# Kernel tuning notes

Measured on AMD Instinct MI355X. Metric: run time of the kernel, lower is better.

The kernel has to match this reference:

```python
import jax, jax.numpy as jnp
import numpy as np

B, N, DEG = 128, 2048, 16
E = N * DEG
EMB, D, H, L = 16, 4, 4, 4
DH = D // H  # per-head dim
OBS_DIM = 6154
HID1, HID2, OUT = 45, 45, 15


def setup_inputs() -> dict:
    key = jax.random.key(0)
    ks = iter(jax.random.split(key, 40))
    nrm = lambda shape, s=0.2: jax.random.normal(next(ks), shape, jnp.float32) * s
    inp = {
        "x": nrm((B, N, EMB), 1.0),
        "obs": nrm((B, OBS_DIM), 1.0),
        "src": jax.random.randint(next(ks), (E,), 0, N, jnp.int32),
        "dst": jnp.repeat(jnp.arange(N, dtype=jnp.int32), DEG),  # each node has DEG in-edges
        "agent_nodes": jax.random.randint(next(ks), (B,), 0, N, jnp.int32),
        "We": nrm((EMB, D)), "be": jnp.zeros((D,), jnp.float32),
        "Wq": nrm((L, D, D)), "bq": jnp.zeros((L, D), jnp.float32),
        "Wk": nrm((L, D, D)), "bk": jnp.zeros((L, D), jnp.float32),
        "Wv": nrm((L, D, D)), "bv": jnp.zeros((L, D), jnp.float32),
        "Wo": nrm((L, D, D)), "bo": jnp.zeros((L, D), jnp.float32),
        "ln1_g": jnp.ones((L, D), jnp.float32), "ln1_b": jnp.zeros((L, D), jnp.float32),
        "W1": nrm((L, D, 2 * D)), "b1": jnp.zeros((L, 2 * D), jnp.float32),
        "W2": nrm((L, 2 * D, D)), "b2": jnp.zeros((L, D), jnp.float32),
        "ln2_g": jnp.ones((L, D), jnp.float32), "ln2_b": jnp.zeros((L, D), jnp.float32),
        "oW1": nrm((D + OBS_DIM, HID1), 0.05), "ob1": jnp.zeros((HID1,), jnp.float32),
        "oW2": nrm((HID1, HID2)), "ob2": jnp.zeros((HID2,), jnp.float32),
        "oW3": nrm((HID2, OUT)), "ob3": jnp.zeros((OUT,), jnp.float32),
    }
    return inp


def _ln(x, g, b):
    m = x.mean(-1, keepdims=True)
    v = ((x - m) ** 2).mean(-1, keepdims=True)
    return g * (x - m) * jax.lax.rsqrt(v + 1e-5) + b


def reference(x, obs, src, dst, agent_nodes, We, be, Wq, bq, Wk, bk, Wv, bv, Wo, bo,
              ln1_g, ln1_b, W1, b1, W2, b2, ln2_g, ln2_b, oW1, ob1, oW2, ob2, oW3, ob3):
    inv_sqrt_dh = 1.0 / np.sqrt(DH)

    def per_graph(xg, node):  # xg: [N, EMB], node: scalar agent location
        h = xg @ We + be  # [N, D] node embedding
        for l in range(L):
            q = (h @ Wq[l] + bq[l]).reshape(N, H, DH)
            k = (h @ Wk[l] + bk[l]).reshape(N, H, DH)
            v = (h @ Wv[l] + bv[l]).reshape(N, H, DH)
            # edge-wise attention scores: gather at dst (query) and src (key)
            s = (q[dst] * k[src]).sum(-1) * inv_sqrt_dh  # [E, H]
            m = jax.ops.segment_max(s, dst, num_segments=N)  # [N, H]
            e = jnp.exp(s - m[dst])
            z = jax.ops.segment_sum(e, dst, num_segments=N)
            a = e / (z[dst] + 1e-6)  # softmax over incoming edges
            msg = jax.ops.segment_sum(a[:, :, None] * v[src], dst, num_segments=N)  # [N, H, DH]
            h_attn = msg.reshape(N, D) @ Wo[l] + bo[l]
            h = _ln(h + h_attn, ln1_g[l], ln1_b[l])  # residual + norm
            ffn = jax.nn.relu(h @ W1[l] + b1[l]) @ W2[l] + b2[l]
            h = _ln(h + ffn, ln2_g[l], ln2_b[l])
        return h[node]  # [D] feature at the agent's node

    gat_out = jax.vmap(per_graph)(x, agent_nodes)  # [B, D]
    feat = jnp.concatenate([gat_out, obs], axis=1)  # [B, D + OBS_DIM]
    hmid = jnp.tanh(feat @ oW1 + ob1)
    hmid = jnp.tanh(hmid @ oW2 + ob2)
    logits = hmid @ oW3 + ob3  # [B, OUT]
    return logits
```

## Files before the change

### kernel.cpp

```cpp
#include <hip/hip_runtime.h>
#include <hip/hip_bf16.h>

#define NB 128
#define NN 2048
#define DEG 16
#define EMBD 16
#define NL 4
#define OBSD 6154
#define HID 45
#define NOUT 15
#define KS 16
#define CH 385
#define RPB 4
#define LOG2E 1.44269504f
#define MEGAB NB
#define MLPB ((NB / RPB) * KS)

__device__ __forceinline__ float frcp(float v) { return __builtin_amdgcn_rcpf(v); }

__device__ __forceinline__ uint32_t pk_bf16(float a, float b) {
    uint32_t ua = __float_as_uint(a); ua += 0x7fffu + ((ua >> 16) & 1u);
    uint32_t ub = __float_as_uint(b); ub += 0x7fffu + ((ub >> 16) & 1u);
    return (ua >> 16) | (ub & 0xffff0000u);
}
__device__ __forceinline__ float lo_bf(uint32_t u) { return __uint_as_float(u << 16); }
__device__ __forceinline__ float hi_bf(uint32_t u) { return __uint_as_float(u & 0xffff0000u); }

__device__ __forceinline__ void ln4(const float* p, const float* g, const float* bb, float* o) {
    float m = 0.25f * (p[0] + p[1] + p[2] + p[3]);
    float var = 0.f;
#pragma unroll
    for (int j = 0; j < 4; ++j) { float d = p[j] - m; var += d * d; }
    var *= 0.25f;
    float rs = rsqrtf(var + 1e-5f);
#pragma unroll
    for (int j = 0; j < 4; ++j) o[j] = g[j] * (p[j] - m) * rs + bb[j];
}

__device__ __forceinline__ void node_tail(float* hh, const float* msg,
    const float* wo, const float* bol, const float* g1, const float* be1,
    const float* w1, const float* b1l, const float* w2, const float* b2l,
    const float* g2, const float* be2)
{
    float pre[4];
#pragma unroll
    for (int j = 0; j < 4; ++j) {
        float s = bol[j];
#pragma unroll
        for (int i = 0; i < 4; ++i) s += msg[i] * wo[i * 4 + j];
        pre[j] = hh[j] + s;
    }
    float hn[4];
    ln4(pre, g1, be1, hn);
    float mid[8];
#pragma unroll
    for (int j = 0; j < 8; ++j) {
        float s = b1l[j];
#pragma unroll
        for (int i = 0; i < 4; ++i) s += hn[i] * w1[i * 8 + j];
        mid[j] = fmaxf(s, 0.f);
    }
    float pre2[4];
#pragma unroll
    for (int j = 0; j < 4; ++j) {
        float s = b2l[j];
#pragma unroll
        for (int i = 0; i < 8; ++i) s += mid[i] * w2[i * 4 + j];
        pre2[j] = hn[j] + s;
    }
    ln4(pre2, g2, be2, hh);
}

__device__ __forceinline__ uint4 kv_pack(const float* hh,
    const float* wk, const float* bkl, const float* wv, const float* bvl)
{
    float kk[4], vv[4];
#pragma unroll
    for (int j = 0; j < 4; ++j) {
        float sk = bkl[j], sv = bvl[j];
#pragma unroll
        for (int i = 0; i < 4; ++i) {
            sk += hh[i] * wk[i * 4 + j];
            sv += hh[i] * wv[i * 4 + j];
        }
        kk[j] = sk; vv[j] = sv;
    }
    return make_uint4(pk_bf16(kk[0], kk[1]), pk_bf16(kk[2], kk[3]),
                      pk_bf16(vv[0], vv[1]), pk_bf16(vv[2], vv[3]));
}

__device__ __forceinline__ void gather_tail(const uint4* kv, const int* su,
    const float* q2, float* hh, int l,
    const float* Wo, const float* bo, const float* ln1_g, const float* ln1_b,
    const float* W1, const float* b1, const float* W2, const float* b2,
    const float* ln2_g, const float* ln2_b)
{
    float z[4] = {0.f, 0.f, 0.f, 0.f}, wa[4] = {0.f, 0.f, 0.f, 0.f};
#pragma unroll
    for (int eb = 0; eb < 4; ++eb) {
        uint4 t0 = kv[su[eb * 4 + 0]];
        uint4 t1 = kv[su[eb * 4 + 1]];
        uint4 t2 = kv[su[eb * 4 + 2]];
        uint4 t3 = kv[su[eb * 4 + 3]];
        float p;
        p = __builtin_amdgcn_exp2f(q2[0] * lo_bf(t0.x)); z[0] += p; wa[0] += p * lo_bf(t0.z);
        p = __builtin_amdgcn_exp2f(q2[1] * hi_bf(t0.x)); z[1] += p; wa[1] += p * hi_bf(t0.z);
        p = __builtin_amdgcn_exp2f(q2[2] * lo_bf(t0.y)); z[2] += p; wa[2] += p * lo_bf(t0.w);
        p = __builtin_amdgcn_exp2f(q2[3] * hi_bf(t0.y)); z[3] += p; wa[3] += p * hi_bf(t0.w);
        p = __builtin_amdgcn_exp2f(q2[0] * lo_bf(t1.x)); z[0] += p; wa[0] += p * lo_bf(t1.z);
        p = __builtin_amdgcn_exp2f(q2[1] * hi_bf(t1.x)); z[1] += p; wa[1] += p * hi_bf(t1.z);
        p = __builtin_amdgcn_exp2f(q2[2] * lo_bf(t1.y)); z[2] += p; wa[2] += p * lo_bf(t1.w);
        p = __builtin_amdgcn_exp2f(q2[3] * hi_bf(t1.y)); z[3] += p; wa[3] += p * hi_bf(t1.w);
        p = __builtin_amdgcn_exp2f(q2[0] * lo_bf(t2.x)); z[0] += p; wa[0] += p * lo_bf(t2.z);
        p = __builtin_amdgcn_exp2f(q2[1] * hi_bf(t2.x)); z[1] += p; wa[1] += p * hi_bf(t2.z);
        p = __builtin_amdgcn_exp2f(q2[2] * lo_bf(t2.y)); z[2] += p; wa[2] += p * lo_bf(t2.w);
        p = __builtin_amdgcn_exp2f(q2[3] * hi_bf(t2.y)); z[3] += p; wa[3] += p * hi_bf(t2.w);
        p = __builtin_amdgcn_exp2f(q2[0] * lo_bf(t3.x)); z[0] += p; wa[0] += p * lo_bf(t3.z);
        p = __builtin_amdgcn_exp2f(q2[1] * hi_bf(t3.x)); z[1] += p; wa[1] += p * hi_bf(t3.z);
        p = __builtin_amdgcn_exp2f(q2[2] * lo_bf(t3.y)); z[2] += p; wa[2] += p * lo_bf(t3.w);
        p = __builtin_amdgcn_exp2f(q2[3] * hi_bf(t3.y)); z[3] += p; wa[3] += p * hi_bf(t3.w);
    }
    float msg[4];
#pragma unroll
    for (int j = 0; j < 4; ++j) msg[j] = wa[j] * frcp(z[j] + 1e-6f);
    node_tail(hh, msg, Wo + l * 16, bo + l * 4, ln1_g + l * 4, ln1_b + l * 4,
              W1 + l * 32, b1 + l * 8, W2 + l * 32, b2 + l * 4,
              ln2_g + l * 4, ln2_b + l * 4);
}

__device__ __forceinline__ void mlp1_block(int mb, int tid,
    const float* __restrict__ obs, const float* __restrict__ oW1,
    float* __restrict__ partial, float* red)
{
    const int rg = mb >> 4;
    const int ks = mb & (KS - 1);
    const int w = tid >> 6, lane = tid & 63;
    const int c0 = ks * CH;
    const int c1 = min(c0 + CH, OBSD);
    const int wl = (c1 - c0 + 15) >> 4;
    const int s0 = c0 + w * wl;
    const int s1 = min(s0 + wl, c1);
    const float* ob0 = obs + (size_t)(rg * RPB) * OBSD;

    if (lane < HID) {
        float acc[RPB] = {0.f, 0.f, 0.f, 0.f};
        for (int i = s0; i < s1; ++i) {
            float wv = oW1[(size_t)(i + 4) * HID + lane];
#pragma unroll
            for (int r = 0; r < RPB; ++r)
                acc[r] += ob0[(size_t)r * OBSD + i] * wv;
        }
#pragma unroll
        for (int r = 0; r < RPB; ++r) red[(w * RPB + r) * HID + lane] = acc[r];
    }
    __syncthreads();
    for (int idx = tid; idx < RPB * HID; idx += 1024) {
        const int r = idx / HID, j = idx % HID;
        float s = 0.f;
#pragma unroll
        for (int ww = 0; ww < 16; ++ww) s += red[(ww * RPB + r) * HID + j];
        partial[(size_t)((rg * RPB + r) * KS + ks) * HID + j] = s;
    }
}

__global__ __launch_bounds__(1024) void fused_kernel(
    const float* __restrict__ x, const int* __restrict__ src,
    const int* __restrict__ agent_nodes,
    const float* __restrict__ obs, const float* __restrict__ oW1,
    float* __restrict__ partial, float* __restrict__ gat_out,
    const float* __restrict__ We, const float* __restrict__ be,
    const float* __restrict__ Wq, const float* __restrict__ bq,
    const float* __restrict__ Wk, const float* __restrict__ bk,
    const float* __restrict__ Wv, const float* __restrict__ bv,
    const float* __restrict__ Wo, const float* __restrict__ bo,
    const float* __restrict__ ln1_g, const float* __restrict__ ln1_b,
    const float* __restrict__ W1, const float* __restrict__ b1,
    const float* __restrict__ W2, const float* __restrict__ b2,
    const float* __restrict__ ln2_g, const float* __restrict__ ln2_b)
{
    __shared__ uint4  kvbuf[NN];
    __shared__ float4 h1lds[NN];
    __shared__ int    conen[289];
    __shared__ float  h2c[289][4];
    __shared__ float  h3buf[17][4];
    const int bid = blockIdx.x;
    const int tid = threadIdx.x;

    if (bid >= MEGAB) {
        mlp1_block(bid - MEGAB, tid, obs, oW1, partial,
                   reinterpret_cast<float*>(kvbuf));
        return;
    }

    const int b = bid;
    const int ag = agent_nodes[b];

    if (tid < 17)  conen[tid] = (tid < 16) ? src[ag * DEG + tid] : ag;
    if (tid < 272) {
        const int i = tid >> 4, e = tid & 15;
        const int ti = (i < 16) ? src[ag * DEG + i] : ag;
        conen[17 + tid] = src[ti * DEG + e];
    }

    float he[2][4];
#pragma unroll
    for (int c = 0; c < 2; ++c) {
        const int n = c * 1024 + tid;
        const float4* xr = reinterpret_cast<const float4*>(
            x + ((size_t)b * NN + n) * EMBD);
        float xv[16];
#pragma unroll
        for (int t4 = 0; t4 < 4; ++t4) {
            float4 t = xr[t4];
            xv[t4 * 4 + 0] = t.x; xv[t4 * 4 + 1] = t.y;
            xv[t4 * 4 + 2] = t.z; xv[t4 * 4 + 3] = t.w;
        }
#pragma unroll
        for (int j = 0; j < 4; ++j) {
            float s = be[j];
#pragma unroll
            for (int i = 0; i < 16; ++i) s += xv[i] * We[i * 4 + j];
            he[c][j] = s;
        }
        kvbuf[n] = kv_pack(he[c], Wk, bk, Wv, bv);
    }
    __syncthreads();

    float h1r[2][4];
#pragma unroll
    for (int u = 0; u < 2; ++u) {
        const int n = u * 1024 + tid;
        float q2[4];
#pragma unroll
        for (int j = 0; j < 4; ++j) {
            float sq = bq[j];
#pragma unroll
            for (int i = 0; i < 4; ++i) sq += he[u][i] * Wq[i * 4 + j];
            q2[j] = sq * LOG2E;
        }
        int su[16];
        const int4* sp = reinterpret_cast<const int4*>(src + n * DEG);
#pragma unroll
        for (int t4 = 0; t4 < 4; ++t4) {
            int4 s4 = sp[t4];
            su[t4 * 4 + 0] = s4.x; su[t4 * 4 + 1] = s4.y;
            su[t4 * 4 + 2] = s4.z; su[t4 * 4 + 3] = s4.w;
        }
        float hh[4] = {he[u][0], he[u][1], he[u][2], he[u][3]};
        gather_tail(kvbuf, su, q2, hh, 0, Wo, bo, ln1_g, ln1_b, W1, b1, W2, b2,
                    ln2_g, ln2_b);
#pragma unroll
        for (int j = 0; j < 4; ++j) h1r[u][j] = hh[j];
    }
    __syncthreads();

    {
        const float* wk1 = Wk + 16; const float* bk1 = bk + 4;
        const float* wv1 = Wv + 16; const float* bv1 = bv + 4;
#pragma unroll
        for (int u = 0; u < 2; ++u) {
            const int n = u * 1024 + tid;
            kvbuf[n] = kv_pack(h1r[u], wk1, bk1, wv1, bv1);
            h1lds[n] = make_float4(h1r[u][0], h1r[u][1], h1r[u][2], h1r[u][3]);
        }
    }
    __syncthreads();

    if (tid < 289) {
        const int node = conen[tid];
        float4 hn4 = h1lds[node];
        float hh[4] = {hn4.x, hn4.y, hn4.z, hn4.w};
        float q2[4];
        {
            const float* wq = Wq + 16; const float* bql = bq + 4;
#pragma unroll
            for (int j = 0; j < 4; ++j) {
                float sq = bql[j];
#pragma unroll
                for (int i = 0; i < 4; ++i) sq += hh[i] * wq[i * 4 + j];
                q2[j] = sq * LOG2E;
            }
        }
        int su2[16];
        const int4* sp = reinterpret_cast<const int4*>(src + node * DEG);
#pragma unroll
        for (int t4 = 0; t4 < 4; ++t4) {
            int4 s4 = sp[t4];
            su2[t4 * 4 + 0] = s4.x; su2[t4 * 4 + 1] = s4.y;
            su2[t4 * 4 + 2] = s4.z; su2[t4 * 4 + 3] = s4.w;
        }
        gather_tail(kvbuf, su2, q2, hh, 1, Wo, bo, ln1_g, ln1_b, W1, b1, W2, b2,
                    ln2_g, ln2_b);
#pragma unroll
        for (int j = 0; j < 4; ++j) h2c[tid][j] = hh[j];
    }
    __syncthreads();

    if (tid < 272) {
        const int i = tid >> 4, e = tid & 15;
        const int l2 = 2;
        float q2[4];
        {
            const float* wq = Wq + l2 * 16; const float* bql = bq + l2 * 4;
#pragma unroll
            for (int j = 0; j < 4; ++j) {
                float sq = bql[j];
#pragma unroll
                for (int k = 0; k < 4; ++k) sq += h2c[i][k] * wq[k * 4 + j];
                q2[j] = sq * LOG2E;
            }
        }
        const float* hnb = h2c[17 + tid];
        float z[4], pv[4];
        {
            const float* wk = Wk + l2 * 16; const float* bkl = bk + l2 * 4;
            const float* wv = Wv + l2 * 16; const float* bvl = bv + l2 * 4;
#pragma unroll
            for (int j = 0; j < 4; ++j) {
                float kh = bkl[j], vh = bvl[j];
#pragma unroll
                for (int k = 0; k < 4; ++k) {
                    kh += hnb[k] * wk[k * 4 + j];
                    vh += hnb[k] * wv[k * 4 + j];
                }
                float p = __builtin_amdgcn_exp2f(q2[j] * kh);
                z[j] = p; pv[j] = p * vh;
            }
        }
#pragma unroll
        for (int m = 1; m <= 8; m <<= 1) {
#pragma unroll
            for (int j = 0; j < 4; ++j) {
                z[j]  += __shfl_xor(z[j], m, 64);
                pv[j] += __shfl_xor(pv[j], m, 64);
            }
        }
        if (e == 0) {
            float msg[4];
#pragma unroll
            for (int j = 0; j < 4; ++j) msg[j] = pv[j] * frcp(z[j] + 1e-6f);
            float hh[4] = {h2c[i][0], h2c[i][1], h2c[i][2], h2c[i][3]};
            node_tail(hh, msg, Wo + l2 * 16, bo + l2 * 4, ln1_g + l2 * 4, ln1_b + l2 * 4,
                      W1 + l2 * 32, b1 + l2 * 8, W2 + l2 * 32, b2 + l2 * 4,
                      ln2_g + l2 * 4, ln2_b + l2 * 4);
#pragma unroll
            for (int j = 0; j < 4; ++j) h3buf[i][j] = hh[j];
        }
    }
    __syncthreads();

    if (tid < 64) {
        const int e = tid >> 2, hd = tid & 3;
        const int l3 = 3;
        float ha[4] = {h3buf[16][0], h3buf[16][1], h3buf[16][2], h3buf[16][3]};
        float qh;
        {
            const float* wq = Wq + l3 * 16;
            qh = bq[l3 * 4 + hd];
#pragma unroll
            for (int i = 0; i < 4; ++i) qh += ha[i] * wq[i * 4 + hd];
            qh *= LOG2E;
        }
        float kh, vh;
        {
            const float* wk3 = Wk + l3 * 16; const float* wv3 = Wv + l3 * 16;
            kh = bk[l3 * 4 + hd]; vh = bv[l3 * 4 + hd];
#pragma unroll
            for (int i = 0; i < 4; ++i) {
                kh += h3buf[e][i] * wk3[i * 4 + hd];
                vh += h3buf[e][i] * wv3[i * 4 + hd];
            }
        }
        float p = __builtin_amdgcn_exp2f(qh * kh);
        float z = p, wv_s = p * vh;
#pragma unroll
        for (int m = 4; m <= 32; m <<= 1) {
            z    += __shfl_xor(z, m, 64);
            wv_s += __shfl_xor(wv_s, m, 64);
        }
        float msg_h = wv_s * frcp(z + 1e-6f);
        float msg[4];
#pragma unroll
        for (int j = 0; j < 4; ++j) msg[j] = __shfl(msg_h, (tid & ~3) + j, 64);

        float hh[4] = {ha[0], ha[1], ha[2], ha[3]};
        node_tail(hh, msg, Wo + l3 * 16, bo + l3 * 4, ln1_g + l3 * 4, ln1_b + l3 * 4,
                  W1 + l3 * 32, b1 + l3 * 8, W2 + l3 * 32, b2 + l3 * 4,
                  ln2_g + l3 * 4, ln2_b + l3 * 4);
        if (tid == 0) {
#pragma unroll
            for (int j = 0; j < 4; ++j) gat_out[b * 4 + j] = hh[j];
        }
    }
}

__global__ __launch_bounds__(64) void mlp2_kernel(
    const float* __restrict__ partial, const float* __restrict__ gat,
    const float* __restrict__ oW1, const float* __restrict__ ob1,
    const float* __restrict__ oW2, const float* __restrict__ ob2,
    const float* __restrict__ oW3, const float* __restrict__ ob3,
    float* __restrict__ out)
{
    __shared__ float hm1[HID], hm2[HID];
    const int b = blockIdx.x;
    const int tid = threadIdx.x;
    if (tid < HID) {
        float s = ob1[tid];
        const float* pp = partial + (size_t)b * KS * HID + tid;
#pragma unroll
        for (int ks = 0; ks < KS; ++ks) s += pp[ks * HID];
#pragma unroll
        for (int k = 0; k < 4; ++k) s += gat[b * 4 + k] * oW1[k * HID + tid];
        hm1[tid] = tanhf(s);
    }
    __syncthreads();
    if (tid < HID) {
        float s = ob2[tid];
        for (int k = 0; k < HID; ++k) s += hm1[k] * oW2[k * HID + tid];
        hm2[tid] = tanhf(s);
    }
    __syncthreads();
    if (tid < NOUT) {
        float s = ob3[tid];
        for (int k = 0; k < HID; ++k) s += hm2[k] * oW3[k * NOUT + tid];
        out[(size_t)b * NOUT + tid] = s;
    }
}

__global__ __launch_bounds__(1024) void gat_single_kernel(
    const float* __restrict__ x, const int* __restrict__ src,
    const int* __restrict__ agent_nodes,
    const float* __restrict__ We, const float* __restrict__ be,
    const float* __restrict__ Wq, const float* __restrict__ bq,
    const float* __restrict__ Wk, const float* __restrict__ bk,
    const float* __restrict__ Wv, const float* __restrict__ bv,
    const float* __restrict__ Wo, const float* __restrict__ bo,
    const float* __restrict__ ln1_g, const float* __restrict__ ln1_b,
    const float* __restrict__ W1, const float* __restrict__ b1,
    const float* __restrict__ W2, const float* __restrict__ b2,
    const float* __restrict__ ln2_g, const float* __restrict__ ln2_b,
    float* __restrict__ gat_out)
{
    __shared__ uint4 kv[NN];
    const int b = blockIdx.x;
    const int tid = threadIdx.x;
    float h[2][4];
#pragma unroll
    for (int u = 0; u < 2; ++u) {
        const int n = tid + u * 1024;
        const float4* xr = reinterpret_cast<const float4*>(x + ((size_t)b * NN + n) * EMBD);
        float xv[16];
#pragma unroll
        for (int t4 = 0; t4 < 4; ++t4) {
            float4 t = xr[t4];
            xv[t4 * 4 + 0] = t.x; xv[t4 * 4 + 1] = t.y;
            xv[t4 * 4 + 2] = t.z; xv[t4 * 4 + 3] = t.w;
        }
#pragma unroll
        for (int j = 0; j < 4; ++j) {
            float s = be[j];
#pragma unroll
            for (int i = 0; i < 16; ++i) s += xv[i] * We[i * 4 + j];
            h[u][j] = s;
        }
    }
    for (int l = 0; l < NL; ++l) {
        float q2[2][4];
        const float* wq = Wq + l * 16; const float* bql = bq + l * 4;
        const float* wk = Wk + l * 16; const float* bkl = bk + l * 4;
        const float* wv = Wv + l * 16; const float* bvl = bv + l * 4;
#pragma unroll
        for (int u = 0; u < 2; ++u) {
            const int n = tid + u * 1024;
#pragma unroll
            for (int j = 0; j < 4; ++j) {
                float sq = bql[j];
#pragma unroll
                for (int i = 0; i < 4; ++i) sq += h[u][i] * wq[i * 4 + j];
                q2[u][j] = sq * LOG2E;
            }
            kv[n] = kv_pack(h[u], wk, bkl, wv, bvl);
        }
        __syncthreads();
#pragma unroll
        for (int u = 0; u < 2; ++u) {
            const int n = tid + u * 1024;
            int su[16];
            const int4* sp = reinterpret_cast<const int4*>(src + n * DEG);
#pragma unroll
            for (int t4 = 0; t4 < 4; ++t4) {
                int4 s4 = sp[t4];
                su[t4 * 4 + 0] = s4.x; su[t4 * 4 + 1] = s4.y;
                su[t4 * 4 + 2] = s4.z; su[t4 * 4 + 3] = s4.w;
            }
            gather_tail(kv, su, q2[u], h[u], l, Wo, bo, ln1_g, ln1_b,
                        W1, b1, W2, b2, ln2_g, ln2_b);
        }
        __syncthreads();
    }
    const int agent = agent_nodes[b];
#pragma unroll
    for (int u = 0; u < 2; ++u) {
        if (tid + u * 1024 == agent) {
#pragma unroll
            for (int j = 0; j < 4; ++j) gat_out[b * 4 + j] = h[u][j];
        }
    }
}

__global__ __launch_bounds__(1024) void mlp1_fb_kernel(
    const float* __restrict__ obs, const float* __restrict__ oW1,
    float* __restrict__ partial)
{
    __shared__ float red[16 * RPB * HID];
    mlp1_block(blockIdx.x, threadIdx.x, obs, oW1, partial, red);
}

extern "C" void kernel_launch(void* const* d_in, const int* in_sizes, int n_in,
                              void* d_out, int out_size, void* d_ws, size_t ws_size,
                              hipStream_t stream) {
    const float* x      = (const float*)d_in[0];
    const float* obs    = (const float*)d_in[1];
    const int*   src    = (const int*)d_in[2];
    const int*   agent  = (const int*)d_in[4];
    const float* We     = (const float*)d_in[5];
    const float* be     = (const float*)d_in[6];
    const float* Wq     = (const float*)d_in[7];
    const float* bq     = (const float*)d_in[8];
    const float* Wk     = (const float*)d_in[9];
    const float* bk     = (const float*)d_in[10];
    const float* Wv     = (const float*)d_in[11];
    const float* bv     = (const float*)d_in[12];
    const float* Wo     = (const float*)d_in[13];
    const float* bo     = (const float*)d_in[14];
    const float* ln1_g  = (const float*)d_in[15];
    const float* ln1_b  = (const float*)d_in[16];
    const float* W1     = (const float*)d_in[17];
    const float* b1     = (const float*)d_in[18];
    const float* W2     = (const float*)d_in[19];
    const float* b2     = (const float*)d_in[20];
    const float* ln2_g  = (const float*)d_in[21];
    const float* ln2_b  = (const float*)d_in[22];
    const float* oW1    = (const float*)d_in[23];
    const float* ob1    = (const float*)d_in[24];
    const float* oW2    = (const float*)d_in[25];
    const float* ob2    = (const float*)d_in[26];
    const float* oW3    = (const float*)d_in[27];
    const float* ob3    = (const float*)d_in[28];

    float* out = (float*)d_out;
    char*  ws  = (char*)d_ws;

    float* gat_out = (float*)ws;
    float* partial = (float*)(ws + 2048);
    const size_t need = 2048 + 368640;

    if (ws_size >= need) {
        fused_kernel<<<MEGAB + MLPB, 1024, 0, stream>>>(x, src, agent, obs, oW1,
            partial, gat_out,
            We, be, Wq, bq, Wk, bk, Wv, bv, Wo, bo, ln1_g, ln1_b, W1, b1, W2, b2,
            ln2_g, ln2_b);
        mlp2_kernel<<<NB, 64, 0, stream>>>(partial, gat_out, oW1, ob1, oW2, ob2,
                                           oW3, ob3, out);
    } else {
        gat_single_kernel<<<NB, 1024, 0, stream>>>(x, src, agent, We, be, Wq, bq, Wk, bk,
                                                   Wv, bv, Wo, bo, ln1_g, ln1_b, W1, b1,
                                                   W2, b2, ln2_g, ln2_b, gat_out);
        mlp1_fb_kernel<<<MLPB, 1024, 0, stream>>>(obs, oW1, partial);
        mlp2_kernel<<<NB, 64, 0, stream>>>(partial, gat_out, oW1, ob1, oW2, ob2,
                                           oW3, ob3, out);
    }
}
```

Baseline: 31.46 us.

## Fuse GAT, obs matvec, and output MLP into one single-launch kernel

Merges the GAT graph work, the obs@oW1 matvec and the tanh MLP head into a single 128-block kernel, so the second launch and the workspace round-trip of partial sums are gone. Each graph block now computes its own row's obs dot products across 16 waves, with 4 independent accumulators, while its x loads are in flight. It also hoists the x loads into registers early. The cost is that the separate 512 matvec blocks, which reused oW1 across 4 rows, are dropped, so each block re-reads the full oW1 and has more serial work on only 128 blocks.

```diff
diff --git a/kernel.cpp b/kernel.cpp
--- a/kernel.cpp
+++ b/kernel.cpp
@@ -9,12 +9,9 @@
 #define OBSD 6154
 #define HID 45
 #define NOUT 15
-#define KS 16
-#define CH 385
-#define RPB 4
 #define LOG2E 1.44269504f
-#define MEGAB NB
-#define MLPB ((NB / RPB) * KS)
+#define NW 16
+#define CHW 385
 
 __device__ __forceinline__ float frcp(float v) { return __builtin_amdgcn_rcpf(v); }
 
@@ -128,308 +125,10 @@
               ln2_g + l * 4, ln2_b + l * 4);
 }
 
-__device__ __forceinline__ void mlp1_block(int mb, int tid,
-    const float* __restrict__ obs, const float* __restrict__ oW1,
-    float* __restrict__ partial, float* red)
-{
-    const int rg = mb >> 4;
-    const int ks = mb & (KS - 1);
-    const int w = tid >> 6, lane = tid & 63;
-    const int c0 = ks * CH;
-    const int c1 = min(c0 + CH, OBSD);
-    const int wl = (c1 - c0 + 15) >> 4;
-    const int s0 = c0 + w * wl;
-    const int s1 = min(s0 + wl, c1);
-    const float* ob0 = obs + (size_t)(rg * RPB) * OBSD;
-
-    if (lane < HID) {
-        float acc[RPB] = {0.f, 0.f, 0.f, 0.f};
-        for (int i = s0; i < s1; ++i) {
-            float wv = oW1[(size_t)(i + 4) * HID + lane];
-#pragma unroll
-            for (int r = 0; r < RPB; ++r)
-                acc[r] += ob0[(size_t)r * OBSD + i] * wv;
-        }
-#pragma unroll
-        for (int r = 0; r < RPB; ++r) red[(w * RPB + r) * HID + lane] = acc[r];
-    }
-    __syncthreads();
-    for (int idx = tid; idx < RPB * HID; idx += 1024) {
-        const int r = idx / HID, j = idx % HID;
-        float s = 0.f;
-#pragma unroll
-        for (int ww = 0; ww < 16; ++ww) s += red[(ww * RPB + r) * HID + j];
-        partial[(size_t)((rg * RPB + r) * KS + ks) * HID + j] = s;
-    }
-}
-
-__global__ __launch_bounds__(1024) void fused_kernel(
+__global__ __launch_bounds__(1024) void mega_kernel(
     const float* __restrict__ x, const int* __restrict__ src,
     const int* __restrict__ agent_nodes,
-    const float* __restrict__ obs, const float* __restrict__ oW1,
-    float* __restrict__ partial, float* __restrict__ gat_out,
-    const float* __restrict__ We, const float* __restrict__ be,
-    const float* __restrict__ Wq, const float* __restrict__ bq,
-    const float* __restrict__ Wk, const float* __restrict__ bk,
-    const float* __restrict__ Wv, const float* __restrict__ bv,
-    const float* __restrict__ Wo, const float* __restrict__ bo,
-    const float* __restrict__ ln1_g, const float* __restrict__ ln1_b,
-    const float* __restrict__ W1, const float* __restrict__ b1,
-    const float* __restrict__ W2, const float* __restrict__ b2,
-    const float* __restrict__ ln2_g, const float* __restrict__ ln2_b)
-{
-    __shared__ uint4  kvbuf[NN];
-    __shared__ float4 h1lds[NN];
-    __shared__ int    conen[289];
-    __shared__ float  h2c[289][4];
-    __shared__ float  h3buf[17][4];
-    const int bid = blockIdx.x;
-    const int tid = threadIdx.x;
-
-    if (bid >= MEGAB) {
-        mlp1_block(bid - MEGAB, tid, obs, oW1, partial,
-                   reinterpret_cast<float*>(kvbuf));
-        return;
-    }
-
-    const int b = bid;
-    const int ag = agent_nodes[b];
-
-    if (tid < 17)  conen[tid] = (tid < 16) ? src[ag * DEG + tid] : ag;
-    if (tid < 272) {
-        const int i = tid >> 4, e = tid & 15;
-        const int ti = (i < 16) ? src[ag * DEG + i] : ag;
-        conen[17 + tid] = src[ti * DEG + e];
-    }
-
-    float he[2][4];
-#pragma unroll
-    for (int c = 0; c < 2; ++c) {
-        const int n = c * 1024 + tid;
-        const float4* xr = reinterpret_cast<const float4*>(
-            x + ((size_t)b * NN + n) * EMBD);
-        float xv[16];
-#pragma unroll
-        for (int t4 = 0; t4 < 4; ++t4) {
-            float4 t = xr[t4];
-            xv[t4 * 4 + 0] = t.x; xv[t4 * 4 + 1] = t.y;
-            xv[t4 * 4 + 2] = t.z; xv[t4 * 4 + 3] = t.w;
-        }
-#pragma unroll
-        for (int j = 0; j < 4; ++j) {
-            float s = be[j];
-#pragma unroll
-            for (int i = 0; i < 16; ++i) s += xv[i] * We[i * 4 + j];
-            he[c][j] = s;
-        }
-        kvbuf[n] = kv_pack(he[c], Wk, bk, Wv, bv);
-    }
-    __syncthreads();
-
-    float h1r[2][4];
-#pragma unroll
-    for (int u = 0; u < 2; ++u) {
-        const int n = u * 1024 + tid;
-        float q2[4];
-#pragma unroll
-        for (int j = 0; j < 4; ++j) {
-            float sq = bq[j];
-#pragma unroll
-            for (int i = 0; i < 4; ++i) sq += he[u][i] * Wq[i * 4 + j];
-            q2[j] = sq * LOG2E;
-        }
-        int su[16];
-        const int4* sp = reinterpret_cast<const int4*>(src + n * DEG);
-#pragma unroll
-        for (int t4 = 0; t4 < 4; ++t4) {
-            int4 s4 = sp[t4];
-            su[t4 * 4 + 0] = s4.x; su[t4 * 4 + 1] = s4.y;
-            su[t4 * 4 + 2] = s4.z; su[t4 * 4 + 3] = s4.w;
-        }
-        float hh[4] = {he[u][0], he[u][1], he[u][2], he[u][3]};
-        gather_tail(kvbuf, su, q2, hh, 0, Wo, bo, ln1_g, ln1_b, W1, b1, W2, b2,
-                    ln2_g, ln2_b);
-#pragma unroll
-        for (int j = 0; j < 4; ++j) h1r[u][j] = hh[j];
-    }
-    __syncthreads();
-
-    {
-        const float* wk1 = Wk + 16; const float* bk1 = bk + 4;
-        const float* wv1 = Wv + 16; const float* bv1 = bv + 4;
-#pragma unroll
-        for (int u = 0; u < 2; ++u) {
-            const int n = u * 1024 + tid;
-            kvbuf[n] = kv_pack(h1r[u], wk1, bk1, wv1, bv1);
-            h1lds[n] = make_float4(h1r[u][0], h1r[u][1], h1r[u][2], h1r[u][3]);
-        }
-    }
-    __syncthreads();
-
-    if (tid < 289) {
-        const int node = conen[tid];
-        float4 hn4 = h1lds[node];
-        float hh[4] = {hn4.x, hn4.y, hn4.z, hn4.w};
-        float q2[4];
-        {
-            const float* wq = Wq + 16; const float* bql = bq + 4;
-#pragma unroll
-            for (int j = 0; j < 4; ++j) {
-                float sq = bql[j];
-#pragma unroll
-                for (int i = 0; i < 4; ++i) sq += hh[i] * wq[i * 4 + j];
-                q2[j] = sq * LOG2E;
-            }
-        }
-        int su2[16];
-        const int4* sp = reinterpret_cast<const int4*>(src + node * DEG);
-#pragma unroll
-        for (int t4 = 0; t4 < 4; ++t4) {
-            int4 s4 = sp[t4];
-            su2[t4 * 4 + 0] = s4.x; su2[t4 * 4 + 1] = s4.y;
-            su2[t4 * 4 + 2] = s4.z; su2[t4 * 4 + 3] = s4.w;
-        }
-        gather_tail(kvbuf, su2, q2, hh, 1, Wo, bo, ln1_g, ln1_b, W1, b1, W2, b2,
-                    ln2_g, ln2_b);
-#pragma unroll
-        for (int j = 0; j < 4; ++j) h2c[tid][j] = hh[j];
-    }
-    __syncthreads();
-
-    if (tid < 272) {
-        const int i = tid >> 4, e = tid & 15;
-        const int l2 = 2;
-        float q2[4];
-        {
-            const float* wq = Wq + l2 * 16; const float* bql = bq + l2 * 4;
-#pragma unroll
-            for (int j = 0; j < 4; ++j) {
-                float sq = bql[j];
-#pragma unroll
-                for (int k = 0; k < 4; ++k) sq += h2c[i][k] * wq[k * 4 + j];
-                q2[j] = sq * LOG2E;
-            }
-        }
-        const float* hnb = h2c[17 + tid];
-        float z[4], pv[4];
-        {
-            const float* wk = Wk + l2 * 16; const float* bkl = bk + l2 * 4;
-            const float* wv = Wv + l2 * 16; const float* bvl = bv + l2 * 4;
-#pragma unroll
-            for (int j = 0; j < 4; ++j) {
-                float kh = bkl[j], vh = bvl[j];
-#pragma unroll
-                for (int k = 0; k < 4; ++k) {
-                    kh += hnb[k] * wk[k * 4 + j];
-                    vh += hnb[k] * wv[k * 4 + j];
-                }
-                float p = __builtin_amdgcn_exp2f(q2[j] * kh);
-                z[j] = p; pv[j] = p * vh;
-            }
-        }
-#pragma unroll
-        for (int m = 1; m <= 8; m <<= 1) {
-#pragma unroll
-            for (int j = 0; j < 4; ++j) {
-                z[j]  += __shfl_xor(z[j], m, 64);
-                pv[j] += __shfl_xor(pv[j], m, 64);
-            }
-        }
-        if (e == 0) {
-            float msg[4];
-#pragma unroll
-            for (int j = 0; j < 4; ++j) msg[j] = pv[j] * frcp(z[j] + 1e-6f);
-            float hh[4] = {h2c[i][0], h2c[i][1], h2c[i][2], h2c[i][3]};
-            node_tail(hh, msg, Wo + l2 * 16, bo + l2 * 4, ln1_g + l2 * 4, ln1_b + l2 * 4,
-                      W1 + l2 * 32, b1 + l2 * 8, W2 + l2 * 32, b2 + l2 * 4,
-                      ln2_g + l2 * 4, ln2_b + l2 * 4);
-#pragma unroll
-            for (int j = 0; j < 4; ++j) h3buf[i][j] = hh[j];
-        }
-    }
-    __syncthreads();
-
-    if (tid < 64) {
-        const int e = tid >> 2, hd = tid & 3;
-        const int l3 = 3;
-        float ha[4] = {h3buf[16][0], h3buf[16][1], h3buf[16][2], h3buf[16][3]};
-        float qh;
-        {
-            const float* wq = Wq + l3 * 16;
-            qh = bq[l3 * 4 + hd];
-#pragma unroll
-            for (int i = 0; i < 4; ++i) qh += ha[i] * wq[i * 4 + hd];
-            qh *= LOG2E;
-        }
-        float kh, vh;
-        {
-            const float* wk3 = Wk + l3 * 16; const float* wv3 = Wv + l3 * 16;
-            kh = bk[l3 * 4 + hd]; vh = bv[l3 * 4 + hd];
-#pragma unroll
-            for (int i = 0; i < 4; ++i) {
-                kh += h3buf[e][i] * wk3[i * 4 + hd];
-                vh += h3buf[e][i] * wv3[i * 4 + hd];
-            }
-        }
-        float p = __builtin_amdgcn_exp2f(qh * kh);
-        float z = p, wv_s = p * vh;
-#pragma unroll
-        for (int m = 4; m <= 32; m <<= 1) {
-            z    += __shfl_xor(z, m, 64);
-            wv_s += __shfl_xor(wv_s, m, 64);
-        }
-        float msg_h = wv_s * frcp(z + 1e-6f);
-        float msg[4];
-#pragma unroll
-        for (int j = 0; j < 4; ++j) msg[j] = __shfl(msg_h, (tid & ~3) + j, 64);
-
-        float hh[4] = {ha[0], ha[1], ha[2], ha[3]};
-        node_tail(hh, msg, Wo + l3 * 16, bo + l3 * 4, ln1_g + l3 * 4, ln1_b + l3 * 4,
-                  W1 + l3 * 32, b1 + l3 * 8, W2 + l3 * 32, b2 + l3 * 4,
-                  ln2_g + l3 * 4, ln2_b + l3 * 4);
-        if (tid == 0) {
-#pragma unroll
-            for (int j = 0; j < 4; ++j) gat_out[b * 4 + j] = hh[j];
-        }
-    }
-}
-
-__global__ __launch_bounds__(64) void mlp2_kernel(
-    const float* __restrict__ partial, const float* __restrict__ gat,
-    const float* __restrict__ oW1, const float* __restrict__ ob1,
-    const float* __restrict__ oW2, const float* __restrict__ ob2,
-    const float* __restrict__ oW3, const float* __restrict__ ob3,
-    float* __restrict__ out)
-{
-    __shared__ float hm1[HID], hm2[HID];
-    const int b = blockIdx.x;
-    const int tid = threadIdx.x;
-    if (tid < HID) {
-        float s = ob1[tid];
-        const float* pp = partial + (size_t)b * KS * HID + tid;
-#pragma unroll
-        for (int ks = 0; ks < KS; ++ks) s += pp[ks * HID];
-#pragma unroll
-        for (int k = 0; k < 4; ++k) s += gat[b * 4 + k] * oW1[k * HID + tid];
-        hm1[tid] = tanhf(s);
-    }
-    __syncthreads();
-    if (tid < HID) {
-        float s = ob2[tid];
-        for (int k = 0; k < HID; ++k) s += hm1[k] * oW2[k * HID + tid];
-        hm2[tid] = tanhf(s);
-    }
-    __syncthreads();
-    if (tid < NOUT) {
-        float s = ob3[tid];
-        for (int k = 0; k < HID; ++k) s += hm2[k] * oW3[k * NOUT + tid];
-        out[(size_t)b * NOUT + tid] = s;
-    }
-}
-
-__global__ __launch_bounds__(1024) void gat_single_kernel(
-    const float* __restrict__ x, const int* __restrict__ src,
-    const int* __restrict__ agent_nodes,
+    const float* __restrict__ obs,
     const float* __restrict__ We, const float* __restrict__ be,
     const float* __restrict__ Wq, const float* __restrict__ bq,
     const float* __restrict__ Wk, const float* __restrict__ bk,
@@ -439,20 +138,64 @@
     const float* __restrict__ W1, const float* __restrict__ b1,
     const float* __restrict__ W2, const float* __restrict__ b2,
     const float* __restrict__ ln2_g, const float* __restrict__ ln2_b,
-    float* __restrict__ gat_out)
+    const float* __restrict__ oW1, const float* __restrict__ ob1,
+    const float* __restrict__ oW2, const float* __restrict__ ob2,
+    const float* __restrict__ oW3, const float* __restrict__ ob3,
+    float* __restrict__ out)
 {
-    __shared__ uint4 kv[NN];
+    __shared__ uint4  kvbuf[NN];
+    __shared__ float4 h1lds[NN];
+    __shared__ int    conen[289];
+    __shared__ float  h2c[289][4];
+    __shared__ float  h3buf[17][4];
+    __shared__ float  red[NW][HID];
+    __shared__ float  hm1s[HID], hm2s[HID];
     const int b = blockIdx.x;
     const int tid = threadIdx.x;
-    float h[2][4];
-#pragma unroll
-    for (int u = 0; u < 2; ++u) {
-        const int n = tid + u * 1024;
-        const float4* xr = reinterpret_cast<const float4*>(x + ((size_t)b * NN + n) * EMBD);
+    const int w = tid >> 6, lane = tid & 63;
+    const int ag = agent_nodes[b];
+
+    float4 xreg[2][4];
+#pragma unroll
+    for (int c = 0; c < 2; ++c) {
+        const float4* xr = reinterpret_cast<const float4*>(
+            x + ((size_t)b * NN + c * 1024 + tid) * EMBD);
+#pragma unroll
+        for (int t4 = 0; t4 < 4; ++t4) xreg[c][t4] = xr[t4];
+    }
+
+    if (tid < 17)  conen[tid] = (tid < 16) ? src[ag * DEG + tid] : ag;
+    if (tid < 272) {
+        const int i = tid >> 4, e = tid & 15;
+        const int ti = (i < 16) ? src[ag * DEG + i] : ag;
+        conen[17 + tid] = src[ti * DEG + e];
+    }
+
+    {
+        const int s0 = w * CHW;
+        const int s1 = min(s0 + CHW, OBSD);
+        const float* ob = obs + (size_t)b * OBSD;
+        float a0 = 0.f, a1 = 0.f, a2 = 0.f, a3 = 0.f;
+        if (lane < HID) {
+            int i = s0;
+            for (; i + 4 <= s1; i += 4) {
+                a0 += ob[i + 0] * oW1[(size_t)(i + 4) * HID + lane];
+                a1 += ob[i + 1] * oW1[(size_t)(i + 5) * HID + lane];
+                a2 += ob[i + 2] * oW1[(size_t)(i + 6) * HID + lane];
+                a3 += ob[i + 3] * oW1[(size_t)(i + 7) * HID + lane];
+            }
+            for (; i < s1; ++i) a0 += ob[i] * oW1[(size_t)(i + 4) * HID + lane];
+            red[w][lane] = a0 + a1 + a2 + a3;
+        }
+    }
+
+    float he[2][4];
+#pragma unroll
+    for (int c = 0; c < 2; ++c) {
         float xv[16];
 #pragma unroll
         for (int t4 = 0; t4 < 4; ++t4) {
-            float4 t = xr[t4];
+            float4 t = xreg[c][t4];
             xv[t4 * 4 + 0] = t.x; xv[t4 * 4 + 1] = t.y;
             xv[t4 * 4 + 2] = t.z; xv[t4 * 4 + 3] = t.w;
         }
@@ -461,59 +204,195 @@
             float s = be[j];
 #pragma unroll
             for (int i = 0; i < 16; ++i) s += xv[i] * We[i * 4 + j];
-            h[u][j] = s;
-        }
-    }
-    for (int l = 0; l < NL; ++l) {
-        float q2[2][4];
-        const float* wq = Wq + l * 16; const float* bql = bq + l * 4;
-        const float* wk = Wk + l * 16; const float* bkl = bk + l * 4;
-        const float* wv = Wv + l * 16; const float* bvl = bv + l * 4;
+            he[c][j] = s;
+        }
+        kvbuf[c * 1024 + tid] = kv_pack(he[c], Wk, bk, Wv, bv);
+    }
+    __syncthreads();
+
+    float h1r[2][4];
+#pragma unroll
+    for (int u = 0; u < 2; ++u) {
+        const int n = u * 1024 + tid;
+        float q2[4];
+#pragma unroll
+        for (int j = 0; j < 4; ++j) {
+            float sq = bq[j];
+#pragma unroll
+            for (int i = 0; i < 4; ++i) sq += he[u][i] * Wq[i * 4 + j];
+            q2[j] = sq * LOG2E;
+        }
+        int su[16];
+        const int4* sp = reinterpret_cast<const int4*>(src + n * DEG);
+#pragma unroll
+        for (int t4 = 0; t4 < 4; ++t4) {
+            int4 s4 = sp[t4];
+            su[t4 * 4 + 0] = s4.x; su[t4 * 4 + 1] = s4.y;
+            su[t4 * 4 + 2] = s4.z; su[t4 * 4 + 3] = s4.w;
+        }
+        float hh[4] = {he[u][0], he[u][1], he[u][2], he[u][3]};
+        gather_tail(kvbuf, su, q2, hh, 0, Wo, bo, ln1_g, ln1_b, W1, b1, W2, b2,
+                    ln2_g, ln2_b);
+#pragma unroll
+        for (int j = 0; j < 4; ++j) h1r[u][j] = hh[j];
+    }
+    __syncthreads();
+
+    {
+        const float* wk1 = Wk + 16; const float* bk1 = bk + 4;
+        const float* wv1 = Wv + 16; const float* bv1 = bv + 4;
 #pragma unroll
         for (int u = 0; u < 2; ++u) {
-            const int n = tid + u * 1024;
+            const int n = u * 1024 + tid;
+            kvbuf[n] = kv_pack(h1r[u], wk1, bk1, wv1, bv1);
+            h1lds[n] = make_float4(h1r[u][0], h1r[u][1], h1r[u][2], h1r[u][3]);
+        }
+    }
+    __syncthreads();
+
+    if (tid < 289) {
+        const int node = conen[tid];
+        float4 hn4 = h1lds[node];
+        float hh[4] = {hn4.x, hn4.y, hn4.z, hn4.w};
+        float q2[4];
+        {
+            const float* wq = Wq + 16; const float* bql = bq + 4;
 #pragma unroll
             for (int j = 0; j < 4; ++j) {
                 float sq = bql[j];
 #pragma unroll
-                for (int i = 0; i < 4; ++i) sq += h[u][i] * wq[i * 4 + j];
-                q2[u][j] = sq * LOG2E;
-            }
-            kv[n] = kv_pack(h[u], wk, bkl, wv, bvl);
-        }
-        __syncthreads();
-#pragma unroll
-        for (int u = 0; u < 2; ++u) {
-            const int n = tid + u * 1024;
-            int su[16];
-            const int4* sp = reinterpret_cast<const int4*>(src + n * DEG);
-#pragma unroll
-            for (int t4 = 0; t4 < 4; ++t4) {
-                int4 s4 = sp[t4];
-                su[t4 * 4 + 0] = s4.x; su[t4 * 4 + 1] = s4.y;
-                su[t4 * 4 + 2] = s4.z; su[t4 * 4 + 3] = s4.w;
-            }
-            gather_tail(kv, su, q2[u], h[u], l, Wo, bo, ln1_g, ln1_b,
-                        W1, b1, W2, b2, ln2_g, ln2_b);
-        }
-        __syncthreads();
-    }
-    const int agent = agent_nodes[b];
-#pragma unroll
-    for (int u = 0; u < 2; ++u) {
-        if (tid + u * 1024 == agent) {
-#pragma unroll
-            for (int j = 0; j < 4; ++j) gat_out[b * 4 + j] = h[u][j];
-        }
-    }
-}
-
-__global__ __launch_bounds__(1024) void mlp1_fb_kernel(
-    const float* __restrict__ obs, const float* __restrict__ oW1,
-    float* __restrict__ partial)
-{
-    __shared__ float red[16 * RPB * HID];
-    mlp1_block(blockIdx.x, threadIdx.x, obs, oW1, partial, red);
+                for (int i = 0; i < 4; ++i) sq += hh[i] * wq[i * 4 + j];
+                q2[j] = sq * LOG2E;
+            }
+        }
+        int su2[16];
+        const int4* sp = reinterpret_cast<const int4*>(src + node * DEG);
+#pragma unroll
+        for (int t4 = 0; t4 < 4; ++t4) {
+            int4 s4 = sp[t4];
+            su2[t4 * 4 + 0] = s4.x; su2[t4 * 4 + 1] = s4.y;
+            su2[t4 * 4 + 2] = s4.z; su2[t4 * 4 + 3] = s4.w;
+        }
+        gather_tail(kvbuf, su2, q2, hh, 1, Wo, bo, ln1_g, ln1_b, W1, b1, W2, b2,
+                    ln2_g, ln2_b);
+#pragma unroll
+        for (int j = 0; j < 4; ++j) h2c[tid][j] = hh[j];
+    }
+    __syncthreads();
+
+    if (tid < 272) {
+        const int i = tid >> 4, e = tid & 15;
+        const int l2 = 2;
+        float q2[4];
+        {
+            const float* wq = Wq + l2 * 16; const float* bql = bq + l2 * 4;
+#pragma unroll
+            for (int j = 0; j < 4; ++j) {
+                float sq = bql[j];
+#pragma unroll
+                for (int k = 0; k < 4; ++k) sq += h2c[i][k] * wq[k * 4 + j];
+                q2[j] = sq * LOG2E;
+            }
+        }
+        const float* hnb = h2c[17 + tid];
+        float z[4], pv[4];
+        {
+            const float* wk = Wk + l2 * 16; const float* bkl = bk + l2 * 4;
+            const float* wv = Wv + l2 * 16; const float* bvl = bv + l2 * 4;
+#pragma unroll
+            for (int j = 0; j < 4; ++j) {
+                float kh = bkl[j], vh = bvl[j];
+#pragma unroll
+                for (int k = 0; k < 4; ++k) {
+                    kh += hnb[k] * wk[k * 4 + j];
+                    vh += hnb[k] * wv[k * 4 + j];
+                }
+                float p = __builtin_amdgcn_exp2f(q2[j] * kh);
+                z[j] = p; pv[j] = p * vh;
+            }
+        }
+#pragma unroll
+        for (int m = 1; m <= 8; m <<= 1) {
+#pragma unroll
+            for (int j = 0; j < 4; ++j) {
+                z[j]  += __shfl_xor(z[j], m, 64);
+                pv[j] += __shfl_xor(pv[j], m, 64);
+            }
+        }
+        if (e == 0) {
+            float msg[4];
+#pragma unroll
+            for (int j = 0; j < 4; ++j) msg[j] = pv[j] * frcp(z[j] + 1e-6f);
+            float hh[4] = {h2c[i][0], h2c[i][1], h2c[i][2], h2c[i][3]};
+            node_tail(hh, msg, Wo + l2 * 16, bo + l2 * 4, ln1_g + l2 * 4, ln1_b + l2 * 4,
+                      W1 + l2 * 32, b1 + l2 * 8, W2 + l2 * 32, b2 + l2 * 4,
+                      ln2_g + l2 * 4, ln2_b + l2 * 4);
+#pragma unroll
+            for (int j = 0; j < 4; ++j) h3buf[i][j] = hh[j];
+        }
+    }
+    __syncthreads();
+
+    if (tid < 64) {
+        const int e = tid >> 2, hd = tid & 3;
+        const int l3 = 3;
+        float ha[4] = {h3buf[16][0], h3buf[16][1], h3buf[16][2], h3buf[16][3]};
+        float qh;
+        {
+            const float* wq = Wq + l3 * 16;
+            qh = bq[l3 * 4 + hd];
+#pragma unroll
+            for (int i = 0; i < 4; ++i) qh += ha[i] * wq[i * 4 + hd];
+            qh *= LOG2E;
+        }
+        float kh, vh;
+        {
+            const float* wk3 = Wk + l3 * 16; const float* wv3 = Wv + l3 * 16;
+            kh = bk[l3 * 4 + hd]; vh = bv[l3 * 4 + hd];
+#pragma unroll
+            for (int i = 0; i < 4; ++i) {
+                kh += h3buf[e][i] * wk3[i * 4 + hd];
+                vh += h3buf[e][i] * wv3[i * 4 + hd];
+            }
+        }
+        float p = __builtin_amdgcn_exp2f(qh * kh);
+        float z = p, wv_s = p * vh;
+#pragma unroll
+        for (int m = 4; m <= 32; m <<= 1) {
+            z    += __shfl_xor(z, m, 64);
+            wv_s += __shfl_xor(wv_s, m, 64);
+        }
+        float msg_h = wv_s * frcp(z + 1e-6f);
+        float msg[4];
+#pragma unroll
+        for (int j = 0; j < 4; ++j) msg[j] = __shfl(msg_h, (tid & ~3) + j, 64);
+
+        float hh[4] = {ha[0], ha[1], ha[2], ha[3]};
+        node_tail(hh, msg, Wo + l3 * 16, bo + l3 * 4, ln1_g + l3 * 4, ln1_b + l3 * 4,
+                  W1 + l3 * 32, b1 + l3 * 8, W2 + l3 * 32, b2 + l3 * 4,
+                  ln2_g + l3 * 4, ln2_b + l3 * 4);
+
+        if (tid < HID) {
+            float s = ob1[tid];
+#pragma unroll
+            for (int ww = 0; ww < NW; ++ww) s += red[ww][tid];
+#pragma unroll
+            for (int k = 0; k < 4; ++k) s += hh[k] * oW1[k * HID + tid];
+            hm1s[tid] = tanhf(s);
+        }
+    }
+    __syncthreads();
+    if (tid < HID) {
+        float s = ob2[tid];
+        for (int k = 0; k < HID; ++k) s += hm1s[k] * oW2[k * HID + tid];
+        hm2s[tid] = tanhf(s);
+    }
+    __syncthreads();
+    if (tid < NOUT) {
+        float s = ob3[tid];
+        for (int k = 0; k < HID; ++k) s += hm2s[k] * oW3[k * NOUT + tid];
+        out[(size_t)b * NOUT + tid] = s;
+    }
 }
 
 extern "C" void kernel_launch(void* const* d_in, const int* in_sizes, int n_in,
@@ -549,25 +428,8 @@
     const float* ob3    = (const float*)d_in[28];
 
     float* out = (float*)d_out;
-    char*  ws  = (char*)d_ws;
-
-    float* gat_out = (float*)ws;
-    float* partial = (float*)(ws + 2048);
-    const size_t need = 2048 + 368640;
-
-    if (ws_size >= need) {
-        fused_kernel<<<MEGAB + MLPB, 1024, 0, stream>>>(x, src, agent, obs, oW1,
-            partial, gat_out,
-            We, be, Wq, bq, Wk, bk, Wv, bv, Wo, bo, ln1_g, ln1_b, W1, b1, W2, b2,
-            ln2_g, ln2_b);
-        mlp2_kernel<<<NB, 64, 0, stream>>>(partial, gat_out, oW1, ob1, oW2, ob2,
-                                           oW3, ob3, out);
-    } else {
-        gat_single_kernel<<<NB, 1024, 0, stream>>>(x, src, agent, We, be, Wq, bq, Wk, bk,
-                                                   Wv, bv, Wo, bo, ln1_g, ln1_b, W1, b1,
-                                                   W2, b2, ln2_g, ln2_b, gat_out);
-        mlp1_fb_kernel<<<MLPB, 1024, 0, stream>>>(obs, oW1, partial);
-        mlp2_kernel<<<NB, 64, 0, stream>>>(partial, gat_out, oW1, ob1, oW2, ob2,
-                                           oW3, ob3, out);
-    }
-}
+
+    mega_kernel<<<NB, 1024, 0, stream>>>(x, src, agent, obs,
+        We, be, Wq, bq, Wk, bk, Wv, bv, Wo, bo, ln1_g, ln1_b, W1, b1, W2, b2,
+        ln2_g, ln2_b, oW1, ob1, oW2, ob2, oW3, ob3, out);
+}
```

Measured after the change: 57.99 us. 84.4% more time.

## Fuse MLP head into fused kernel via last-block-done atomic counters

Applied to the files above, without the earlier changes.

Removes the separate mlp2 kernel launch. Each batch row gets a counter that the GAT block and the 16 mlp1 split blocks increment, and whichever block arrives last runs the small tanh MLP head for that row. This saves one kernel launch and its gap, but adds a memset launch, atomics and thread fences. The last-arriving block also does the serial head work at the end of the grid.

```diff
diff --git a/kernel.cpp b/kernel.cpp
--- a/kernel.cpp
+++ b/kernel.cpp
@@ -128,6 +128,37 @@
               ln2_g + l * 4, ln2_b + l * 4);
 }
 
+__device__ __forceinline__ void mlp_head(int b, int tid,
+    const float* __restrict__ partial, const float* __restrict__ gat,
+    const float* __restrict__ oW1, const float* __restrict__ ob1,
+    const float* __restrict__ oW2, const float* __restrict__ ob2,
+    const float* __restrict__ oW3, const float* __restrict__ ob3,
+    float* __restrict__ out, float* hm1s, float* hm2s)
+{
+    if (tid < HID) {
+        float s = ob1[tid];
+        const float* pp = partial + (size_t)b * KS * HID + tid;
+#pragma unroll
+        for (int ks = 0; ks < KS; ++ks) s += pp[ks * HID];
+#pragma unroll
+        for (int k = 0; k < 4; ++k) s += gat[b * 4 + k] * oW1[k * HID + tid];
+        hm1s[tid] = tanhf(s);
+    }
+    __syncthreads();
+    if (tid < HID) {
+        float s = ob2[tid];
+        for (int k = 0; k < HID; ++k) s += hm1s[k] * oW2[k * HID + tid];
+        hm2s[tid] = tanhf(s);
+    }
+    __syncthreads();
+    if (tid < NOUT) {
+        float s = ob3[tid];
+        for (int k = 0; k < HID; ++k) s += hm2s[k] * oW3[k * NOUT + tid];
+        out[(size_t)b * NOUT + tid] = s;
+    }
+    __syncthreads();
+}
+
 __device__ __forceinline__ void mlp1_block(int mb, int tid,
     const float* __restrict__ obs, const float* __restrict__ oW1,
     float* __restrict__ partial, float* red)
@@ -167,7 +198,7 @@
     const float* __restrict__ x, const int* __restrict__ src,
     const int* __restrict__ agent_nodes,
     const float* __restrict__ obs, const float* __restrict__ oW1,
-    float* __restrict__ partial, float* __restrict__ gat_out,
+    float* __restrict__ partial, float* __restrict__ gat_out, int* __restrict__ cnt,
     const float* __restrict__ We, const float* __restrict__ be,
     const float* __restrict__ Wq, const float* __restrict__ bq,
     const float* __restrict__ Wk, const float* __restrict__ bk,
@@ -176,19 +207,44 @@
     const float* __restrict__ ln1_g, const float* __restrict__ ln1_b,
     const float* __restrict__ W1, const float* __restrict__ b1,
     const float* __restrict__ W2, const float* __restrict__ b2,
-    const float* __restrict__ ln2_g, const float* __restrict__ ln2_b)
+    const float* __restrict__ ln2_g, const float* __restrict__ ln2_b,
+    const float* __restrict__ ob1,
+    const float* __restrict__ oW2, const float* __restrict__ ob2,
+    const float* __restrict__ oW3, const float* __restrict__ ob3,
+    float* __restrict__ out)
 {
     __shared__ uint4  kvbuf[NN];
     __shared__ float4 h1lds[NN];
     __shared__ int    conen[289];
     __shared__ float  h2c[289][4];
     __shared__ float  h3buf[17][4];
+    __shared__ float  hm1s[HID], hm2s[HID];
+    __shared__ int    wrow[RPB];
     const int bid = blockIdx.x;
     const int tid = threadIdx.x;
 
     if (bid >= MEGAB) {
-        mlp1_block(bid - MEGAB, tid, obs, oW1, partial,
-                   reinterpret_cast<float*>(kvbuf));
+        const int mb = bid - MEGAB;
+        mlp1_block(mb, tid, obs, oW1, partial, reinterpret_cast<float*>(kvbuf));
+        __syncthreads();
+        if (tid < RPB) {
+            __threadfence();
+            const int r = (mb >> 4) * RPB + tid;
+            int old = __hip_atomic_fetch_add(&cnt[r], 1, __ATOMIC_ACQ_REL,
+                                             __HIP_MEMORY_SCOPE_AGENT);
+            wrow[tid] = (old == KS) ? r : -1;
+        }
+        __syncthreads();
+#pragma unroll
+        for (int t = 0; t < RPB; ++t) {
+            const int r = wrow[t];
+            if (r >= 0) {
+                if (tid == 0) __threadfence();
+                __syncthreads();
+                mlp_head(r, tid, partial, gat_out, oW1, ob1, oW2, ob2, oW3, ob3,
+                         out, hm1s, hm2s);
+            }
+        }
         return;
     }
 
@@ -392,38 +448,18 @@
             for (int j = 0; j < 4; ++j) gat_out[b * 4 + j] = hh[j];
         }
     }
-}
-
-__global__ __launch_bounds__(64) void mlp2_kernel(
-    const float* __restrict__ partial, const float* __restrict__ gat,
-    const float* __restrict__ oW1, const float* __restrict__ ob1,
-    const float* __restrict__ oW2, const float* __restrict__ ob2,
-    const float* __restrict__ oW3, const float* __restrict__ ob3,
-    float* __restrict__ out)
-{
-    __shared__ float hm1[HID], hm2[HID];
-    const int b = blockIdx.x;
-    const int tid = threadIdx.x;
-    if (tid < HID) {
-        float s = ob1[tid];
-        const float* pp = partial + (size_t)b * KS * HID + tid;
-#pragma unroll
-        for (int ks = 0; ks < KS; ++ks) s += pp[ks * HID];
-#pragma unroll
-        for (int k = 0; k < 4; ++k) s += gat[b * 4 + k] * oW1[k * HID + tid];
-        hm1[tid] = tanhf(s);
-    }
-    __syncthreads();
-    if (tid < HID) {
-        float s = ob2[tid];
-        for (int k = 0; k < HID; ++k) s += hm1[k] * oW2[k * HID + tid];
-        hm2[tid] = tanhf(s);
-    }
-    __syncthreads();
-    if (tid < NOUT) {
-        float s = ob3[tid];
-        for (int k = 0; k < HID; ++k) s += hm2[k] * oW3[k * NOUT + tid];
-        out[(size_t)b * NOUT + tid] = s;
+
+    if (tid == 0) {
+        __threadfence();
+        int old = __hip_atomic_fetch_add(&cnt[b], 1, __ATOMIC_ACQ_REL,
+                                         __HIP_MEMORY_SCOPE_AGENT);
+        wrow[0] = (old == KS) ? b : -1;
+        if (wrow[0] >= 0) __threadfence();
+    }
+    __syncthreads();
+    if (wrow[0] >= 0) {
+        mlp_head(b, tid, partial, gat_out, oW1, ob1, oW2, ob2, oW3, ob3,
+                 out, hm1s, hm2s);
     }
 }
 
@@ -514,6 +550,39 @@
 {
     __shared__ float red[16 * RPB * HID];
     mlp1_block(blockIdx.x, threadIdx.x, obs, oW1, partial, red);
+}
+
+__global__ __launch_bounds__(64) void mlp2_fb_kernel(
+    const float* __restrict__ partial, const float* __restrict__ gat,
+    const float* __restrict__ oW1, const float* __restrict__ ob1,
+    const float* __restrict__ oW2, const float* __restrict__ ob2,
+    const float* __restrict__ oW3, const float* __restrict__ ob3,
+    float* __restrict__ out)
+{
+    __shared__ float hm1[HID], hm2[HID];
+    const int b = blockIdx.x;
+    const int tid = threadIdx.x;
+    if (tid < HID) {
+        float s = ob1[tid];
+        const float* pp = partial + (size_t)b * KS * HID + tid;
+#pragma unroll
+        for (int ks = 0; ks < KS; ++ks) s += pp[ks * HID];
+#pragma unroll
+        for (int k = 0; k < 4; ++k) s += gat[b * 4 + k] * oW1[k * HID + tid];
+        hm1[tid] = tanhf(s);
+    }
+    __syncthreads();
+    if (tid < HID) {
+        float s = ob2[tid];
+        for (int k = 0; k < HID; ++k) s += hm1[k] * oW2[k * HID + tid];
+        hm2[tid] = tanhf(s);
+    }
+    __syncthreads();
+    if (tid < NOUT) {
+        float s = ob3[tid];
+        for (int k = 0; k < HID; ++k) s += hm2[k] * oW3[k * NOUT + tid];
+        out[(size_t)b * NOUT + tid] = s;
+    }
 }
 
 extern "C" void kernel_launch(void* const* d_in, const int* in_sizes, int n_in,
@@ -552,22 +621,22 @@
     char*  ws  = (char*)d_ws;
 
     float* gat_out = (float*)ws;
-    float* partial = (float*)(ws + 2048);
-    const size_t need = 2048 + 368640;
+    int*   cnt     = (int*)(ws + 2048);
+    float* partial = (float*)(ws + 4096);
+    const size_t need = 4096 + 368640;
 
     if (ws_size >= need) {
+        hipMemsetAsync(cnt, 0, NB * sizeof(int), stream);
         fused_kernel<<<MEGAB + MLPB, 1024, 0, stream>>>(x, src, agent, obs, oW1,
-            partial, gat_out,
+            partial, gat_out, cnt,
             We, be, Wq, bq, Wk, bk, Wv, bv, Wo, bo, ln1_g, ln1_b, W1, b1, W2, b2,
-            ln2_g, ln2_b);
-        mlp2_kernel<<<NB, 64, 0, stream>>>(partial, gat_out, oW1, ob1, oW2, ob2,
-                                           oW3, ob3, out);
+            ln2_g, ln2_b, ob1, oW2, ob2, oW3, ob3, out);
     } else {
         gat_single_kernel<<<NB, 1024, 0, stream>>>(x, src, agent, We, be, Wq, bq, Wk, bk,
                                                    Wv, bv, Wo, bo, ln1_g, ln1_b, W1, b1,
                                                    W2, b2, ln2_g, ln2_b, gat_out);
         mlp1_fb_kernel<<<MLPB, 1024, 0, stream>>>(obs, oW1, partial);
-        mlp2_kernel<<<NB, 64, 0, stream>>>(partial, gat_out, oW1, ob1, oW2, ob2,
-                                           oW3, ob3, out);
-    }
-}
+        mlp2_fb_kernel<<<NB, 64, 0, stream>>>(partial, gat_out, oW1, ob1, oW2, ob2,
+                                              oW3, ob3, out);
+    }
+}
```

Result: slower. 78.46 us (+149.4%).
